# Performance work log

Hardware: AMD Instinct MI355X
Metric: run time of the kernel (lower is better)

The kernel has to match this reference:

```python
import jax, jax.numpy as jnp
import numpy as np

B, T, N, F = 4, 24, 1024, 96
H, HD = 3, 32      # spatial GATConv: 3 heads, head-dim 32 (averaged -> 32 per branch, 3 branches -> 96)
GH, GHD = 4, 24    # GroupedGAT: 4 heads concatenated -> 96
E = 8192           # edges per graph


def setup_inputs() -> dict:
    key = jax.random.key(0)
    ks = jax.random.split(key, 24)
    s_in = 1.0 / np.sqrt(F)
    def gat_params(k):
        k1, k2, k3, k4 = jax.random.split(k, 4)
        return (jax.random.normal(k1, (F, H * HD), jnp.float32) * s_in,
                jax.random.normal(k2, (H, HD), jnp.float32) * 0.1,
                jax.random.normal(k3, (H, HD), jnp.float32) * 0.1,
                jax.random.normal(k4, (H, HD), jnp.float32) * 0.02)
    W_d, al_d, ar_d, b_d = gat_params(ks[3])
    W_m, al_m, ar_m, b_m = gat_params(ks[4])
    W_s, al_s, ar_s, b_s = gat_params(ks[5])
    inp = {
        "input": jax.random.normal(ks[0], (B, T, N, F), jnp.float32),
        "spatial_embedding": jax.random.normal(ks[1], (B, T, N, F), jnp.float32),
        "temporal_embedding": jax.random.normal(ks[2], (B, T, N, F), jnp.float32),
        "src_d": jax.random.randint(ks[6], (E,), 0, N, jnp.int32),
        "dst_d": (jnp.arange(E) % N).astype(jnp.int32),
        "src_m": jax.random.randint(ks[7], (E,), 0, N, jnp.int32),
        "dst_m": (jnp.arange(E) % N).astype(jnp.int32),
        "src_s": jax.random.randint(ks[8], (E,), 0, N, jnp.int32),
        "dst_s": (jnp.arange(E) % N).astype(jnp.int32),
        "W_d": W_d, "al_d": al_d, "ar_d": ar_d, "b_d": b_d,
        "W_m": W_m, "al_m": al_m, "ar_m": ar_m, "b_m": b_m,
        "W_s": W_s, "al_s": al_s, "ar_s": ar_s, "b_s": b_s,
        "Wg": jax.random.normal(ks[9], (F, GH * GHD), jnp.float32) * s_in,
        "agl": jax.random.normal(ks[10], (GH, GHD), jnp.float32) * 0.1,
        "agr": jax.random.normal(ks[11], (GH, GHD), jnp.float32) * 0.1,
        "Wf": jax.random.normal(ks[12], (2 * F, F), jnp.float32) * (1.0 / np.sqrt(2 * F)),
        "bf": jnp.zeros((F,), jnp.float32),
    }
    return inp


def _gat(x, src, dst, W, al, ar, b):
    # x: (N, K, F) node features with K = T*B batched feature slots
    K = x.shape[1]
    h = (x @ W).reshape(N, K, H, HD)                       # (N,K,H,HD)
    el = (h * al).sum(-1)                                  # (N,K,H)
    er = (h * ar).sum(-1)
    e = jax.nn.leaky_relu(el[src] + er[dst], 0.2)          # (E,K,H)
    emax = jax.ops.segment_max(e, dst, num_segments=N)
    emax = jnp.where(jnp.isfinite(emax), emax, 0.0)
    ex = jnp.exp(e - emax[dst])
    denom = jax.ops.segment_sum(ex, dst, num_segments=N)
    alpha = ex / (denom[dst] + 1e-9)                       # edge softmax over incoming edges
    out = jax.ops.segment_sum(h[src] * alpha[..., None], dst, num_segments=N)
    return (out + b).mean(2)                               # average heads -> (N,K,HD)


def reference(input, spatial_embedding, temporal_embedding,
              src_d, dst_d, src_m, dst_m, src_s, dst_s,
              W_d, al_d, ar_d, b_d, W_m, al_m, ar_m, b_m, W_s, al_s, ar_s, b_s,
              Wg, agl, agr, Wf, bf):
    # ---------------- SpatialBlock ----------------
    residual_s = input                                     # input_dim == output_dim
    x_in = input + spatial_embedding
    # torch: input.transpose(0,2).reshape(N,-1,F) -> slot order is (t,b)
    x = jnp.transpose(x_in, (2, 1, 0, 3)).reshape(N, T * B, F)
    xd = _gat(x, src_d, dst_d, W_d, al_d, ar_d, b_d)
    xm = _gat(x, src_m, dst_m, W_m, al_m, ar_m, b_m)
    xs = _gat(x, src_s, dst_s, W_s, al_s, ar_s, b_s)
    x_attn = jnp.concatenate([xd, xm, xs], axis=-1)        # (N, T*B, 3*HD=F)
    # torch: transpose(0,1).reshape(batch,T,N,-1)  (keeps original (t,b) slot order quirk)
    x_attn = jnp.transpose(x_attn, (1, 0, 2)).reshape(B, T, N, F)
    cov0 = spatial_embedding[:, 0]                         # (B,N,F)
    attn_S = jax.nn.softmax(cov0 @ jnp.swapaxes(cov0, 1, 2), axis=2)  # (B,N,N)
    # NOTE: embedding_x branch in SpatialBlock is dead code (out is overwritten); skipped.
    spatial = residual_s + x_attn

    # ---------------- TemporalBlock ----------------
    residual_t = input
    xt = jnp.swapaxes(input, 1, 2).reshape(B * N, T, F)    # (B*N, T, F), index k=b*N+n
    # GroupedGAT: dense multi-head GAT over the T=period_num time steps
    hg = (xt @ Wg).reshape(B * N, T, GH, GHD)
    elg = (hg * agl).sum(-1)                               # (BN,T,GH)
    erg = (hg * agr).sum(-1)
    eg = jax.nn.leaky_relu(elg[:, :, None, :] + erg[:, None, :, :], 0.2)  # (BN,Ti,Tj,GH)
    alphag = jax.nn.softmax(eg, axis=2)
    xg = jnp.einsum('kijh,kjhd->kihd', alphag, hg).reshape(B * N, T, GH * GHD)
    covT = temporal_embedding[:, :, 0]                     # (B,T,F)
    attn_T = jax.nn.softmax(covT @ jnp.swapaxes(covT, 1, 2), axis=1)      # softmax over dim=1 as in torch
    # torch: attn.repeat(N,1,1) paired with x of batch index b*N+n -> uses attn[(b*N+n) % B]
    idx = (jnp.arange(B * N) % B)
    emb = jnp.einsum('kij,kjf->kif', attn_T[idx], xt)      # (BN,T,F)
    xg = xg * jax.nn.sigmoid(emb)
    xg = jnp.swapaxes(xg.reshape(B, N, T, F), 1, 2)        # (B,T,N,F)
    temporal = residual_t + xg

    # ---------------- Fusion ----------------
    z = jax.nn.sigmoid(jnp.concatenate([spatial, temporal], axis=-1) @ Wf + bf)
    out = z * spatial + (1.0 - z) * temporal + input
    return out, attn_S
```

## Files before the change

### kernel.cpp

```cpp
#include <hip/hip_runtime.h>
#include <hip/hip_bf16.h>

typedef long long i64;
typedef __attribute__((ext_vector_type(8))) short short8b;
typedef __attribute__((ext_vector_type(4))) short short4b;
typedef __attribute__((ext_vector_type(4))) float f32x4;

union U8 { short8b v; ushort s[8]; };
union U4 { short4b v; ushort s[4]; };

static __device__ __forceinline__ float bs2f(ushort u) {
    union { unsigned int i; float f; } x; x.i = ((unsigned int)u) << 16; return x.f;
}
static __device__ __forceinline__ ushort f2bs(float f) {
    __hip_bfloat16 h = __float2bfloat16(f);
    return *reinterpret_cast<ushort*>(&h);
}
static __device__ __forceinline__ void mfma_bf16(f32x4& acc, short8b a, short8b b) {
    asm volatile("v_mfma_f32_16x16x32_bf16 %0, %1, %2, %0" : "+v"(acc) : "v"(a), "v"(b));
}
static __device__ __forceinline__ void mfma_fence() {
    asm volatile("s_nop 7\n\ts_nop 7\n\ts_nop 7");
}


__global__ __launch_bounds__(256) void prep_weights_kernel(const float* __restrict__ Wd,
                                                           const float* __restrict__ Wm,
                                                           const float* __restrict__ Ws,
                                                           const float* __restrict__ Wg,
                                                           const float* __restrict__ Wf,
                                                           ushort* __restrict__ wtab) {
    int idx = blockIdx.x * 256 + threadIdx.x;
    if (idx < 36864) {
        int w = idx / 9216, rem = idx - w * 9216;
        int c = rem / 96, k = rem - c * 96;
        const float* Wsrc = (w == 0) ? Wd : (w == 1) ? Wm : (w == 2) ? Ws : Wg;
        wtab[w * 9216 + c * 96 + k] = f2bs(Wsrc[k * 96 + c]);
    } else {
        int rem = idx - 36864;
        int c = rem / 192, k = rem - c * 192;
        wtab[36864 + c * 192 + k] = f2bs(Wf[k * 96 + c]);
    }
}

__global__ __launch_bounds__(256) void build_x_kernel(const float* __restrict__ inp,
                                                      const float* __restrict__ spat,
                                                      ushort* __restrict__ x) {
    int i4 = blockIdx.x * 256 + threadIdx.x;
    int q = i4 % 24;
    int r = i4 / 24;
    int n = r & 1023, bt = r >> 10;
    int t = bt % 24, b = bt / 24;
    int k = t * 4 + b;
    float4 a = ((const float4*)inp)[i4];
    float4 s = ((const float4*)spat)[i4];
    U4 u;
    u.s[0] = f2bs(a.x + s.x); u.s[1] = f2bs(a.y + s.y);
    u.s[2] = f2bs(a.z + s.z); u.s[3] = f2bs(a.w + s.w);
    *(short4b*)&x[((i64)((k << 10) | n)) * 96 + q * 4] = u.v;
}

__global__ __launch_bounds__(256) void gemm96_mfma_kernel(const ushort* __restrict__ X,
                                                          const ushort* __restrict__ wt,
                                                          ushort* __restrict__ Ho) {
    __shared__ ushort Xs[128 * 104];
    __shared__ ushort Wt[96 * 104];
    int tid = threadIdx.x;
    i64 row0 = (i64)blockIdx.x * 128;
    for (int i = tid; i < 1152; i += 256) {
        int c = i / 12, kg = i - c * 12;
        *(short8b*)&Wt[c * 104 + kg * 8] = *(const short8b*)&wt[c * 96 + kg * 8];
    }
    for (int i = tid; i < 1536; i += 256) {
        int r = i / 12, q = i - r * 12;
        *(short8b*)&Xs[r * 104 + q * 8] = *(const short8b*)&X[(row0 + r) * 96 + q * 8];
    }
    __syncthreads();
    int wid = tid >> 6, lane = tid & 63;
    int lr = lane & 15, lk = lane >> 4;
    f32x4 acc[2][6];
#pragma unroll
    for (int m = 0; m < 2; ++m)
#pragma unroll
        for (int c = 0; c < 6; ++c) acc[m][c] = (f32x4){0.f, 0.f, 0.f, 0.f};
    const ushort* xa = &Xs[(wid * 32 + lr) * 104 + lk * 8];
    const ushort* wb = &Wt[lr * 104 + lk * 8];
#pragma unroll
    for (int ks = 0; ks < 3; ++ks) {
        short8b a0 = *(const short8b*)(xa + ks * 32);
        short8b a1 = *(const short8b*)(xa + 16 * 104 + ks * 32);
#pragma unroll
        for (int c = 0; c < 6; ++c) {
            short8b b = *(const short8b*)(wb + c * 16 * 104 + ks * 32);
            mfma_bf16(acc[0][c], a0, b);
            mfma_bf16(acc[1][c], a1, b);
        }
    }
    mfma_fence();
#pragma unroll
    for (int m = 0; m < 2; ++m)
#pragma unroll
        for (int c = 0; c < 6; ++c)
#pragma unroll
            for (int r = 0; r < 4; ++r) {
                i64 row = row0 + wid * 32 + m * 16 + lk * 4 + r;
                Ho[row * 96 + c * 16 + lr] = f2bs(acc[m][c][r]);
            }
}

__global__ __launch_bounds__(256) void gemm96_hg_mfma_kernel(const float* __restrict__ inp,
                                                             const ushort* __restrict__ wt,
                                                             ushort* __restrict__ Ho) {
    __shared__ ushort Xs[128 * 104];
    __shared__ ushort Wt[96 * 104];
    int tid = threadIdx.x;
    i64 row0 = (i64)blockIdx.x * 128;
    for (int i = tid; i < 1152; i += 256) {
        int c = i / 12, kg = i - c * 12;
        *(short8b*)&Wt[c * 104 + kg * 8] = *(const short8b*)&wt[c * 96 + kg * 8];
    }
    for (int i = tid; i < 3072; i += 256) {
        int r = i / 24, q = i - r * 24;
        int row = (int)row0 + r;
        int kk = row / 24, t = row - kk * 24;
        int b = kk >> 10, n = kk & 1023;
        float4 v = ((const float4*)inp)[((i64)(((b * 24 + t) << 10) | n)) * 24 + q];
        U4 u;
        u.s[0] = f2bs(v.x); u.s[1] = f2bs(v.y); u.s[2] = f2bs(v.z); u.s[3] = f2bs(v.w);
        *(short4b*)&Xs[r * 104 + q * 4] = u.v;
    }
    __syncthreads();
    int wid = tid >> 6, lane = tid & 63;
    int lr = lane & 15, lk = lane >> 4;
    f32x4 acc[2][6];
#pragma unroll
    for (int m = 0; m < 2; ++m)
#pragma unroll
        for (int c = 0; c < 6; ++c) acc[m][c] = (f32x4){0.f, 0.f, 0.f, 0.f};
    const ushort* xa = &Xs[(wid * 32 + lr) * 104 + lk * 8];
    const ushort* wb = &Wt[lr * 104 + lk * 8];
#pragma unroll
    for (int ks = 0; ks < 3; ++ks) {
        short8b a0 = *(const short8b*)(xa + ks * 32);
        short8b a1 = *(const short8b*)(xa + 16 * 104 + ks * 32);
#pragma unroll
        for (int c = 0; c < 6; ++c) {
            short8b b = *(const short8b*)(wb + c * 16 * 104 + ks * 32);
            mfma_bf16(acc[0][c], a0, b);
            mfma_bf16(acc[1][c], a1, b);
        }
    }
    mfma_fence();
#pragma unroll
    for (int m = 0; m < 2; ++m)
#pragma unroll
        for (int c = 0; c < 6; ++c)
#pragma unroll
            for (int r = 0; r < 4; ++r) {
                i64 row = row0 + wid * 32 + m * 16 + lk * 4 + r;
                Ho[row * 96 + c * 16 + lr] = f2bs(acc[m][c][r]);
            }
}

__global__ __launch_bounds__(256) void eler_kernel(const ushort* __restrict__ H2,
                                                   const float* __restrict__ al,
                                                   const float* __restrict__ ar,
                                                   float* __restrict__ el,
                                                   float* __restrict__ er) {
    int idx = blockIdx.x * 256 + threadIdx.x;
    int kn = idx / 3, h = idx - kn * 3;
    const ushort* hp = H2 + (i64)kn * 96 + h * 32;
    const float* alp = al + h * 32;
    const float* arp = ar + h * 32;
    float a = 0.f, b2 = 0.f;
#pragma unroll
    for (int c8 = 0; c8 < 4; ++c8) {
        short8b v = *(const short8b*)(hp + c8 * 8);
#pragma unroll
        for (int q = 0; q < 8; ++q) {
            float hv = bs2f((ushort)v[q]);
            a += hv * alp[c8 * 8 + q];
            b2 += hv * arp[c8 * 8 + q];
        }
    }
    el[idx] = a;
    er[idx] = b2;
}

__global__ __launch_bounds__(256) void gat_agg_kernel(const ushort* __restrict__ H2,
                                                      const float* __restrict__ el,
                                                      const float* __restrict__ er,
                                                      const int* __restrict__ src,
                                                      const float* __restrict__ bv,
                                                      ushort* __restrict__ xattn,
                                                      int g) {
    int tid = threadIdx.x;
    int pp = tid >> 3, l8 = tid & 7;
    int p = blockIdx.x * 32 + pp;
    int k = p >> 10, n = p & 1023;
    int d0 = l8 * 4;
    int s[8];
#pragma unroll
    for (int j = 0; j < 8; ++j) s[j] = src[n + j * 1024];
    float acc[4] = {0.f, 0.f, 0.f, 0.f};
#pragma unroll
    for (int h = 0; h < 3; ++h) {
        float erv = er[((i64)((k << 10) | n)) * 3 + h];
        float e[8];
        float m = -1e30f;
#pragma unroll
        for (int j = 0; j < 8; ++j) {
            float ev = el[((i64)((k << 10) | s[j])) * 3 + h] + erv;
            ev = ev >= 0.f ? ev : 0.2f * ev;
            e[j] = ev;
            m = fmaxf(m, ev);
        }
        float sum = 0.f;
#pragma unroll
        for (int j = 0; j < 8; ++j) { e[j] = expf(e[j] - m); sum += e[j]; }
        float inv = 1.f / (sum + 1e-9f);
        float o[4] = {0.f, 0.f, 0.f, 0.f};
#pragma unroll
        for (int j = 0; j < 8; ++j) {
            U4 hv; hv.v = *(const short4b*)&H2[((i64)((k << 10) | s[j])) * 96 + h * 32 + d0];
#pragma unroll
            for (int c = 0; c < 4; ++c) o[c] += e[j] * bs2f(hv.s[c]);
        }
#pragma unroll
        for (int c = 0; c < 4; ++c) acc[c] += o[c] * inv + bv[h * 32 + d0 + c];
    }
    U4 u;
#pragma unroll
    for (int c = 0; c < 4; ++c) u.s[c] = f2bs(acc[c] * (1.f / 3.f));
    *(short4b*)&xattn[((i64)((k << 10) | n)) * 96 + g * 32 + d0] = u.v;
}

__global__ __launch_bounds__(256) void attn_scores_kernel(const float* __restrict__ spat,
                                                          float* __restrict__ attnS) {
    int bid = blockIdx.x;
    int b = bid >> 8;
    int i0 = ((bid >> 4) & 15) * 64;
    int j0 = (bid & 15) * 64;
    const float* C = spat + (i64)b * 24 * 1024 * 96;
    __shared__ __align__(16) float As[64 * 100];
    __shared__ __align__(16) float Bs[64 * 100];
    int tid = threadIdx.x;
    float4* As4 = (float4*)As;
    float4* Bs4 = (float4*)Bs;
    const float4* Ai = (const float4*)(C + (i64)i0 * 96);
    const float4* Bj = (const float4*)(C + (i64)j0 * 96);
    for (int i = tid; i < 1536; i += 256) {
        int row = i / 24, q = i - row * 24;
        As4[row * 25 + q] = Ai[i];
        Bs4[row * 25 + q] = Bj[i];
    }
    __syncthreads();
    int tj = tid & 15, ti = tid >> 4;
    float acc[4][4];
#pragma unroll
    for (int r = 0; r < 4; ++r)
#pragma unroll
        for (int s = 0; s < 4; ++s) acc[r][s] = 0.f;
    for (int k4 = 0; k4 < 24; ++k4) {
        float4 a[4], bv[4];
#pragma unroll
        for (int r = 0; r < 4; ++r) a[r] = As4[(ti * 4 + r) * 25 + k4];
#pragma unroll
        for (int s = 0; s < 4; ++s) bv[s] = Bs4[(s * 16 + tj) * 25 + k4];
#pragma unroll
        for (int r = 0; r < 4; ++r)
#pragma unroll
            for (int s = 0; s < 4; ++s)
                acc[r][s] += a[r].x * bv[s].x + a[r].y * bv[s].y + a[r].z * bv[s].z + a[r].w * bv[s].w;
    }
#pragma unroll
    for (int r = 0; r < 4; ++r) {
        i64 orow = ((i64)(b << 10) + i0 + ti * 4 + r) * 1024 + j0;
#pragma unroll
        for (int s = 0; s < 4; ++s) attnS[orow + s * 16 + tj] = acc[r][s];
    }
}

__global__ __launch_bounds__(256) void attn_softmax_kernel(float* __restrict__ attnS) {
    i64 base = (i64)blockIdx.x * 1024;
    float4* row4 = (float4*)(attnS + base);
    int tid = threadIdx.x;
    float4 v = row4[tid];
    __shared__ float red[256];
    float m = fmaxf(fmaxf(v.x, v.y), fmaxf(v.z, v.w));
    red[tid] = m;
    __syncthreads();
    for (int st = 128; st > 0; st >>= 1) {
        if (tid < st) red[tid] = fmaxf(red[tid], red[tid + st]);
        __syncthreads();
    }
    m = red[0];
    __syncthreads();
    v.x = expf(v.x - m); v.y = expf(v.y - m); v.z = expf(v.z - m); v.w = expf(v.w - m);
    red[tid] = v.x + v.y + v.z + v.w;
    __syncthreads();
    for (int st = 128; st > 0; st >>= 1) {
        if (tid < st) red[tid] += red[tid + st];
        __syncthreads();
    }
    float inv = 1.f / red[0];
    v.x *= inv; v.y *= inv; v.z *= inv; v.w *= inv;
    row4[tid] = v;
}

__global__ __launch_bounds__(576) void attn_t_kernel(const float* __restrict__ temp,
                                                     float* __restrict__ attnT) {
    int b = blockIdx.x;
    int tid = threadIdx.x;
    __shared__ float cs[24][96];
    __shared__ float M[24][24];
    for (int i = tid; i < 2304; i += 576) {
        int r = i / 96, f = i - r * 96;
        cs[r][f] = temp[((i64)(b * 24 + r)) * 1024 * 96 + f];
    }
    __syncthreads();
    int i = tid / 24, j = tid - i * 24;
    float s = 0.f;
#pragma unroll
    for (int f = 0; f < 96; ++f) s += cs[i][f] * cs[j][f];
    M[i][j] = s;
    __syncthreads();
    float m = -1e30f;
#pragma unroll
    for (int i2 = 0; i2 < 24; ++i2) m = fmaxf(m, M[i2][j]);
    float sum = 0.f;
#pragma unroll
    for (int i2 = 0; i2 < 24; ++i2) sum += expf(M[i2][j] - m);
    attnT[((i64)b * 24 + i) * 24 + j] = expf(M[i][j] - m) / sum;
}

__global__ __launch_bounds__(192) void temporal_kernel(const float* __restrict__ inp,
                                                       const ushort* __restrict__ hg,
                                                       const float* __restrict__ agl,
                                                       const float* __restrict__ agr,
                                                       const float* __restrict__ attnT,
                                                       ushort* __restrict__ gated) {
    int kk = blockIdx.x;
    int b = kk >> 10, n = kk & 1023;
    __shared__ __align__(16) float hgs[24 * 100];
    __shared__ __align__(16) float xs[24 * 100];
    __shared__ float at[24 * 24];
    __shared__ float elg[24][4], erg[24][4];
    __shared__ float alpha[4][24][24];
    int tid = threadIdx.x;
    for (int i = tid; i < 576; i += 192) {
        int r = i / 24, q = i - r * 24;
        U4 u; u.v = *(const short4b*)&hg[(i64)kk * 2304 + r * 96 + q * 4];
        float4 v;
        v.x = bs2f(u.s[0]); v.y = bs2f(u.s[1]); v.z = bs2f(u.s[2]); v.w = bs2f(u.s[3]);
        *(float4*)&hgs[r * 100 + q * 4] = v;
    }
    for (int i = tid; i < 576; i += 192) {
        int r = i / 24, q = i - r * 24;
        *(float4*)&xs[r * 100 + q * 4] =
            ((const float4*)inp)[(((i64)(b * 24 + r)) << 10 | n) * 24 + q];
    }
    int ib = kk & 3;
    for (int i = tid; i < 576; i += 192) at[i] = attnT[ib * 576 + i];
    __syncthreads();
    if (tid < 96) {
        int i = tid >> 2, g = tid & 3;
        float a = 0.f, r2 = 0.f;
#pragma unroll
        for (int d = 0; d < 24; ++d) {
            float hv = hgs[i * 100 + g * 24 + d];
            a += hv * agl[g * 24 + d];
            r2 += hv * agr[g * 24 + d];
        }
        elg[i][g] = a;
        erg[i][g] = r2;
    }
    __syncthreads();
    if (tid < 96) {
        int i = tid >> 2, g = tid & 3;
        float ev[24];
        float m = -1e30f;
        float eli = elg[i][g];
#pragma unroll
        for (int j = 0; j < 24; ++j) {
            float e = eli + erg[j][g];
            e = e >= 0.f ? e : 0.2f * e;
            ev[j] = e;
            m = fmaxf(m, e);
        }
        float sum = 0.f;
#pragma unroll
        for (int j = 0; j < 24; ++j) { ev[j] = expf(ev[j] - m); sum += ev[j]; }
        float inv = 1.f / sum;
#pragma unroll
        for (int j = 0; j < 24; ++j) alpha[g][i][j] = ev[j] * inv;
    }
    __syncthreads();
#pragma unroll
    for (int s2 = 0; s2 < 3; ++s2) {
        int idx = tid + s2 * 192;
        int i = idx / 24, f4 = idx - i * 24;
        int g = f4 / 6;
        const float* ap = &alpha[g][i][0];
        const float* atp = &at[i * 24];
        float4 xg = {0.f, 0.f, 0.f, 0.f}, emb = {0.f, 0.f, 0.f, 0.f};
#pragma unroll 8
        for (int j = 0; j < 24; ++j) {
            float a = ap[j], w = atp[j];
            float4 h4 = *(const float4*)&hgs[j * 100 + f4 * 4];
            float4 x4 = *(const float4*)&xs[j * 100 + f4 * 4];
            xg.x += a * h4.x; xg.y += a * h4.y; xg.z += a * h4.z; xg.w += a * h4.w;
            emb.x += w * x4.x; emb.y += w * x4.y; emb.z += w * x4.z; emb.w += w * x4.w;
        }
        U4 o;
        o.s[0] = f2bs(xg.x / (1.f + expf(-emb.x)));
        o.s[1] = f2bs(xg.y / (1.f + expf(-emb.y)));
        o.s[2] = f2bs(xg.z / (1.f + expf(-emb.z)));
        o.s[3] = f2bs(xg.w / (1.f + expf(-emb.w)));
        *(short4b*)&gated[(i64)kk * 2304 + i * 96 + f4 * 4] = o.v;
    }
}

__global__ __launch_bounds__(256) void fusion_mfma_kernel(const float* __restrict__ inp,
                                                          const ushort* __restrict__ xattn,
                                                          const ushort* __restrict__ gated,
                                                          const ushort* __restrict__ wtf,
                                                          const float* __restrict__ bfv,
                                                          float* __restrict__ outb) {
    __shared__ ushort Xs[64 * 200];
    __shared__ ushort Wt[96 * 200];
    int tid = threadIdx.x;
    i64 row0 = (i64)blockIdx.x * 64;
    for (int i = tid; i < 2304; i += 256) {
        int c = i / 24, kg = i - c * 24;
        *(short8b*)&Wt[c * 200 + kg * 8] = *(const short8b*)&wtf[c * 192 + kg * 8];
    }
    for (int i = tid; i < 768; i += 256) {
        int r = i / 12, q = i - r * 12;
        i64 grow = row0 + r;
        int n = (int)(grow & 1023);
        int bt = (int)(grow >> 10);
        int t = bt % 24, b = bt / 24;
        float4 iv0 = ((const float4*)inp)[grow * 24 + q * 2];
        float4 iv1 = ((const float4*)inp)[grow * 24 + q * 2 + 1];
        U8 xa; xa.v = *(const short8b*)&xattn[grow * 96 + q * 8];
        U8 gd; gd.v = *(const short8b*)&gated[(((i64)((b << 10) | n)) * 24 + t) * 96 + q * 8];
        float ivf[8] = {iv0.x, iv0.y, iv0.z, iv0.w, iv1.x, iv1.y, iv1.z, iv1.w};
        U8 sp, tm;
#pragma unroll
        for (int j = 0; j < 8; ++j) {
            sp.s[j] = f2bs(ivf[j] + bs2f(xa.s[j]));
            tm.s[j] = f2bs(ivf[j] + bs2f(gd.s[j]));
        }
        *(short8b*)&Xs[r * 200 + q * 8] = sp.v;
        *(short8b*)&Xs[r * 200 + 96 + q * 8] = tm.v;
    }
    __syncthreads();
    int wid = tid >> 6, lane = tid & 63;
    int lr = lane & 15, lk = lane >> 4;
    f32x4 acc[6];
#pragma unroll
    for (int c = 0; c < 6; ++c) acc[c] = (f32x4){0.f, 0.f, 0.f, 0.f};
    const ushort* xa = &Xs[(wid * 16 + lr) * 200 + lk * 8];
    const ushort* wb = &Wt[lr * 200 + lk * 8];
#pragma unroll
    for (int ks = 0; ks < 6; ++ks) {
        short8b a = *(const short8b*)(xa + ks * 32);
#pragma unroll
        for (int c = 0; c < 6; ++c) {
            short8b b = *(const short8b*)(wb + c * 16 * 200 + ks * 32);
            mfma_bf16(acc[c], a, b);
        }
    }
    mfma_fence();
#pragma unroll
    for (int c = 0; c < 6; ++c) {
        int col = c * 16 + lr;
        float bfc = bfv[col];
#pragma unroll
        for (int r = 0; r < 4; ++r) {
            int lrow = wid * 16 + lk * 4 + r;
            i64 grow = row0 + lrow;
            float z = 1.f / (1.f + expf(-(acc[c][r] + bfc)));
            float sp = bs2f(Xs[lrow * 200 + col]);
            float tm = bs2f(Xs[lrow * 200 + 96 + col]);
            float iv = inp[grow * 96 + col];
            outb[grow * 96 + col] = z * sp + (1.f - z) * tm + iv;
        }
    }
}

extern "C" void kernel_launch(void* const* d_in, const int* in_sizes, int n_in,
                              void* d_out, int out_size, void* d_ws, size_t ws_size,
                              hipStream_t stream) {
    const float* input = (const float*)d_in[0];
    const float* spat  = (const float*)d_in[1];
    const float* temp  = (const float*)d_in[2];
    const int* src_d = (const int*)d_in[3];
    const int* src_m = (const int*)d_in[5];
    const int* src_s = (const int*)d_in[7];
    const float* W_d  = (const float*)d_in[9];
    const float* al_d = (const float*)d_in[10];
    const float* ar_d = (const float*)d_in[11];
    const float* b_d  = (const float*)d_in[12];
    const float* W_m  = (const float*)d_in[13];
    const float* al_m = (const float*)d_in[14];
    const float* ar_m = (const float*)d_in[15];
    const float* b_m  = (const float*)d_in[16];
    const float* W_s  = (const float*)d_in[17];
    const float* al_s = (const float*)d_in[18];
    const float* ar_s = (const float*)d_in[19];
    const float* b_s  = (const float*)d_in[20];
    const float* Wg   = (const float*)d_in[21];
    const float* agl  = (const float*)d_in[22];
    const float* agr  = (const float*)d_in[23];
    const float* Wf   = (const float*)d_in[24];
    const float* bf_  = (const float*)d_in[25];

    float* outb  = (float*)d_out;
    float* attnS = outb + 9437184;

    float* wsf = (float*)d_ws;
    ushort* xbf      = (ushort*)wsf;
    ushort* hgbf     = xbf;
    ushort* H2bf     = (ushort*)(wsf + 4718592);
    ushort* gatedbf  = H2bf;
    ushort* xattnbf  = (ushort*)(wsf + 9437184);
    float* el    = wsf + 14155776;
    float* er    = el + 294912;
    float* attnT = er + 294912;
    ushort* wtab = (ushort*)(wsf + 14747904);
    ushort* wt_d = wtab;
    ushort* wt_m = wtab + 9216;
    ushort* wt_s = wtab + 18432;
    ushort* wtg  = wtab + 27648;
    ushort* wtf  = wtab + 36864;

    prep_weights_kernel<<<216, 256, 0, stream>>>(W_d, W_m, W_s, Wg, Wf, wtab);
    build_x_kernel<<<9216, 256, 0, stream>>>(input, spat, xbf);

    const ushort* Wgat[3] = {wt_d, wt_m, wt_s};
    const float* algat[3] = {al_d, al_m, al_s};
    const float* argat[3] = {ar_d, ar_m, ar_s};
    const float* bgat[3] = {b_d, b_m, b_s};
    const int* srcs[3] = {src_d, src_m, src_s};
    for (int g = 0; g < 3; ++g) {
        gemm96_mfma_kernel<<<768, 256, 0, stream>>>(xbf, Wgat[g], H2bf);
        eler_kernel<<<1152, 256, 0, stream>>>(H2bf, algat[g], argat[g], el, er);
        gat_agg_kernel<<<3072, 256, 0, stream>>>(H2bf, el, er, srcs[g], bgat[g],
                                                 xattnbf, g);
    }

    attn_scores_kernel<<<1024, 256, 0, stream>>>(spat, attnS);
    attn_softmax_kernel<<<4096, 256, 0, stream>>>(attnS);

    gemm96_hg_mfma_kernel<<<768, 256, 0, stream>>>(input, wtg, hgbf);
    attn_t_kernel<<<4, 576, 0, stream>>>(temp, attnT);
    temporal_kernel<<<4096, 192, 0, stream>>>(input, hgbf, agl, agr, attnT, gatedbf);
    fusion_mfma_kernel<<<1536, 256, 0, stream>>>(input, xattnbf, gatedbf, wtf, bf_, outb);
}
```

Before: 297.3 us.

## Fold attention-logit projections into the GEMM weights as extra output columns

Precomputes W·a_l and W·a_r as extra weight columns, so the spatial and temporal projection GEMMs emit the el/er logits directly from a seventh MFMA column tile. This removes the three eler_kernel launches and their rereads of the bf16 H tensors, plus the per-block logit dot products in temporal_kernel. In exchange each GEMM does about 1/6 more MFMA work, and the logits are now computed from bf16-rounded folded weights rather than from bf16 H, which shifts numerics slightly. The workspace layout is rearranged so the temporal logit buffers reuse the el region.

```diff
diff --git a/kernel.cpp b/kernel.cpp
--- a/kernel.cpp
+++ b/kernel.cpp
@@ -24,22 +24,47 @@
 }
 
 
-__global__ __launch_bounds__(256) void prep_weights_kernel(const float* __restrict__ Wd,
-                                                           const float* __restrict__ Wm,
-                                                           const float* __restrict__ Ws,
-                                                           const float* __restrict__ Wg,
-                                                           const float* __restrict__ Wf,
-                                                           ushort* __restrict__ wtab) {
+__global__ __launch_bounds__(256) void prep_weights_kernel(
+        const float* __restrict__ Wd, const float* __restrict__ Wm,
+        const float* __restrict__ Ws, const float* __restrict__ Wg,
+        const float* __restrict__ Wf,
+        const float* __restrict__ ald, const float* __restrict__ ard,
+        const float* __restrict__ alm, const float* __restrict__ arm,
+        const float* __restrict__ als, const float* __restrict__ ars,
+        const float* __restrict__ agl, const float* __restrict__ agr,
+        ushort* __restrict__ wtab) {
     int idx = blockIdx.x * 256 + threadIdx.x;
-    if (idx < 36864) {
-        int w = idx / 9216, rem = idx - w * 9216;
+    if (idx >= 61440) return;
+    if (idx < 43008) {
+        int w = idx / 10752, rem = idx - w * 10752;
         int c = rem / 96, k = rem - c * 96;
-        const float* Wsrc = (w == 0) ? Wd : (w == 1) ? Wm : (w == 2) ? Ws : Wg;
-        wtab[w * 9216 + c * 96 + k] = f2bs(Wsrc[k * 96 + c]);
+        float v;
+        if (w < 3) {
+            const float* W = (w == 0) ? Wd : (w == 1) ? Wm : Ws;
+            if (c < 96) {
+                v = W[k * 96 + c];
+            } else {
+                int j = c - 96, h = j >> 1;
+                const float* a = (j & 1) ? ((w == 0) ? ard : (w == 1) ? arm : ars)
+                                         : ((w == 0) ? ald : (w == 1) ? alm : als);
+                v = 0.f;
+                for (int d = 0; d < 32; ++d) v += W[k * 96 + h * 32 + d] * a[h * 32 + d];
+            }
+        } else {
+            if (c < 96) {
+                v = Wg[k * 96 + c];
+            } else {
+                int j = c - 96, g = j & 3;
+                const float* a = (j >> 2) ? agr : agl;
+                v = 0.f;
+                for (int d = 0; d < 24; ++d) v += Wg[k * 96 + g * 24 + d] * a[g * 24 + d];
+            }
+        }
+        wtab[w * 10752 + c * 96 + k] = f2bs(v);
     } else {
-        int rem = idx - 36864;
+        int rem = idx - 43008;
         int c = rem / 192, k = rem - c * 192;
-        wtab[36864 + c * 192 + k] = f2bs(Wf[k * 96 + c]);
+        wtab[43008 + c * 192 + k] = f2bs(Wf[k * 96 + c]);
     }
 }
 
@@ -62,12 +87,14 @@
 
 __global__ __launch_bounds__(256) void gemm96_mfma_kernel(const ushort* __restrict__ X,
                                                           const ushort* __restrict__ wt,
-                                                          ushort* __restrict__ Ho) {
+                                                          ushort* __restrict__ Ho,
+                                                          float* __restrict__ el,
+                                                          float* __restrict__ er) {
     __shared__ ushort Xs[128 * 104];
-    __shared__ ushort Wt[96 * 104];
+    __shared__ ushort Wt[112 * 104];
     int tid = threadIdx.x;
     i64 row0 = (i64)blockIdx.x * 128;
-    for (int i = tid; i < 1152; i += 256) {
+    for (int i = tid; i < 1344; i += 256) {
         int c = i / 12, kg = i - c * 12;
         *(short8b*)&Wt[c * 104 + kg * 8] = *(const short8b*)&wt[c * 96 + kg * 8];
     }
@@ -78,11 +105,11 @@
     __syncthreads();
     int wid = tid >> 6, lane = tid & 63;
     int lr = lane & 15, lk = lane >> 4;
-    f32x4 acc[2][6];
+    f32x4 acc[2][7];
 #pragma unroll
     for (int m = 0; m < 2; ++m)
 #pragma unroll
-        for (int c = 0; c < 6; ++c) acc[m][c] = (f32x4){0.f, 0.f, 0.f, 0.f};
+        for (int c = 0; c < 7; ++c) acc[m][c] = (f32x4){0.f, 0.f, 0.f, 0.f};
     const ushort* xa = &Xs[(wid * 32 + lr) * 104 + lk * 8];
     const ushort* wb = &Wt[lr * 104 + lk * 8];
 #pragma unroll
@@ -90,7 +117,7 @@
         short8b a0 = *(const short8b*)(xa + ks * 32);
         short8b a1 = *(const short8b*)(xa + 16 * 104 + ks * 32);
 #pragma unroll
-        for (int c = 0; c < 6; ++c) {
+        for (int c = 0; c < 7; ++c) {
             short8b b = *(const short8b*)(wb + c * 16 * 104 + ks * 32);
             mfma_bf16(acc[0][c], a0, b);
             mfma_bf16(acc[1][c], a1, b);
@@ -98,7 +125,7 @@
     }
     mfma_fence();
 #pragma unroll
-    for (int m = 0; m < 2; ++m)
+    for (int m = 0; m < 2; ++m) {
 #pragma unroll
         for (int c = 0; c < 6; ++c)
 #pragma unroll
@@ -106,16 +133,28 @@
                 i64 row = row0 + wid * 32 + m * 16 + lk * 4 + r;
                 Ho[row * 96 + c * 16 + lr] = f2bs(acc[m][c][r]);
             }
+        if (lr < 6) {
+            float* dst = (lr & 1) ? er : el;
+            int h = lr >> 1;
+#pragma unroll
+            for (int r = 0; r < 4; ++r) {
+                i64 row = row0 + wid * 32 + m * 16 + lk * 4 + r;
+                dst[row * 3 + h] = acc[m][6][r];
+            }
+        }
+    }
 }
 
 __global__ __launch_bounds__(256) void gemm96_hg_mfma_kernel(const float* __restrict__ inp,
                                                              const ushort* __restrict__ wt,
-                                                             ushort* __restrict__ Ho) {
+                                                             ushort* __restrict__ Ho,
+                                                             float* __restrict__ elg,
+                                                             float* __restrict__ erg) {
     __shared__ ushort Xs[128 * 104];
-    __shared__ ushort Wt[96 * 104];
+    __shared__ ushort Wt[112 * 104];
     int tid = threadIdx.x;
     i64 row0 = (i64)blockIdx.x * 128;
-    for (int i = tid; i < 1152; i += 256) {
+    for (int i = tid; i < 1344; i += 256) {
         int c = i / 12, kg = i - c * 12;
         *(short8b*)&Wt[c * 104 + kg * 8] = *(const short8b*)&wt[c * 96 + kg * 8];
     }
@@ -132,11 +171,11 @@
     __syncthreads();
     int wid = tid >> 6, lane = tid & 63;
     int lr = lane & 15, lk = lane >> 4;
-    f32x4 acc[2][6];
+    f32x4 acc[2][7];
 #pragma unroll
     for (int m = 0; m < 2; ++m)
 #pragma unroll
-        for (int c = 0; c < 6; ++c) acc[m][c] = (f32x4){0.f, 0.f, 0.f, 0.f};
+        for (int c = 0; c < 7; ++c) acc[m][c] = (f32x4){0.f, 0.f, 0.f, 0.f};
     const ushort* xa = &Xs[(wid * 32 + lr) * 104 + lk * 8];
     const ushort* wb = &Wt[lr * 104 + lk * 8];
 #pragma unroll
@@ -144,7 +183,7 @@
         short8b a0 = *(const short8b*)(xa + ks * 32);
         short8b a1 = *(const short8b*)(xa + 16 * 104 + ks * 32);
 #pragma unroll
-        for (int c = 0; c < 6; ++c) {
+        for (int c = 0; c < 7; ++c) {
             short8b b = *(const short8b*)(wb + c * 16 * 104 + ks * 32);
             mfma_bf16(acc[0][c], a0, b);
             mfma_bf16(acc[1][c], a1, b);
@@ -152,7 +191,7 @@
     }
     mfma_fence();
 #pragma unroll
-    for (int m = 0; m < 2; ++m)
+    for (int m = 0; m < 2; ++m) {
 #pragma unroll
         for (int c = 0; c < 6; ++c)
 #pragma unroll
@@ -160,31 +199,16 @@
                 i64 row = row0 + wid * 32 + m * 16 + lk * 4 + r;
                 Ho[row * 96 + c * 16 + lr] = f2bs(acc[m][c][r]);
             }
-}
-
-__global__ __launch_bounds__(256) void eler_kernel(const ushort* __restrict__ H2,
-                                                   const float* __restrict__ al,
-                                                   const float* __restrict__ ar,
-                                                   float* __restrict__ el,
-                                                   float* __restrict__ er) {
-    int idx = blockIdx.x * 256 + threadIdx.x;
-    int kn = idx / 3, h = idx - kn * 3;
-    const ushort* hp = H2 + (i64)kn * 96 + h * 32;
-    const float* alp = al + h * 32;
-    const float* arp = ar + h * 32;
-    float a = 0.f, b2 = 0.f;
-#pragma unroll
-    for (int c8 = 0; c8 < 4; ++c8) {
-        short8b v = *(const short8b*)(hp + c8 * 8);
-#pragma unroll
-        for (int q = 0; q < 8; ++q) {
-            float hv = bs2f((ushort)v[q]);
-            a += hv * alp[c8 * 8 + q];
-            b2 += hv * arp[c8 * 8 + q];
-        }
-    }
-    el[idx] = a;
-    er[idx] = b2;
+        if (lr < 8) {
+            float* dst = (lr >> 2) ? erg : elg;
+            int g = lr & 3;
+#pragma unroll
+            for (int r = 0; r < 4; ++r) {
+                i64 row = row0 + wid * 32 + m * 16 + lk * 4 + r;
+                dst[row * 4 + g] = acc[m][6][r];
+            }
+        }
+    }
 }
 
 __global__ __launch_bounds__(256) void gat_agg_kernel(const ushort* __restrict__ H2,
@@ -336,8 +360,8 @@
 
 __global__ __launch_bounds__(192) void temporal_kernel(const float* __restrict__ inp,
                                                        const ushort* __restrict__ hg,
-                                                       const float* __restrict__ agl,
-                                                       const float* __restrict__ agr,
+                                                       const float* __restrict__ elgb,
+                                                       const float* __restrict__ ergb,
                                                        const float* __restrict__ attnT,
                                                        ushort* __restrict__ gated) {
     int kk = blockIdx.x;
@@ -345,7 +369,8 @@
     __shared__ __align__(16) float hgs[24 * 100];
     __shared__ __align__(16) float xs[24 * 100];
     __shared__ float at[24 * 24];
-    __shared__ float elg[24][4], erg[24][4];
+    __shared__ __align__(16) float elg[24][4];
+    __shared__ __align__(16) float erg[24][4];
     __shared__ float alpha[4][24][24];
     int tid = threadIdx.x;
     for (int i = tid; i < 576; i += 192) {
@@ -362,18 +387,10 @@
     }
     int ib = kk & 3;
     for (int i = tid; i < 576; i += 192) at[i] = attnT[ib * 576 + i];
-    __syncthreads();
-    if (tid < 96) {
-        int i = tid >> 2, g = tid & 3;
-        float a = 0.f, r2 = 0.f;
-#pragma unroll
-        for (int d = 0; d < 24; ++d) {
-            float hv = hgs[i * 100 + g * 24 + d];
-            a += hv * agl[g * 24 + d];
-            r2 += hv * agr[g * 24 + d];
-        }
-        elg[i][g] = a;
-        erg[i][g] = r2;
+    for (int i = tid; i < 48; i += 192) {
+        int r = i >> 1;
+        if (i & 1) *(float4*)&erg[r][0] = ((const float4*)ergb)[(i64)kk * 24 + r];
+        else       *(float4*)&elg[r][0] = ((const float4*)elgb)[(i64)kk * 24 + r];
     }
     __syncthreads();
     if (tid < 96) {
@@ -528,25 +545,26 @@
     ushort* xattnbf  = (ushort*)(wsf + 9437184);
     float* el    = wsf + 14155776;
     float* er    = el + 294912;
-    float* attnT = er + 294912;
-    ushort* wtab = (ushort*)(wsf + 14747904);
+    float* elgb  = wsf + 14155776;
+    float* attnT = wsf + 14745600;
+    float* ergb  = wsf + 14747904;
+    ushort* wtab = (ushort*)(wsf + 15141120);
     ushort* wt_d = wtab;
-    ushort* wt_m = wtab + 9216;
-    ushort* wt_s = wtab + 18432;
-    ushort* wtg  = wtab + 27648;
-    ushort* wtf  = wtab + 36864;
-
-    prep_weights_kernel<<<216, 256, 0, stream>>>(W_d, W_m, W_s, Wg, Wf, wtab);
+    ushort* wt_m = wtab + 10752;
+    ushort* wt_s = wtab + 21504;
+    ushort* wtg  = wtab + 32256;
+    ushort* wtf  = wtab + 43008;
+
+    prep_weights_kernel<<<240, 256, 0, stream>>>(W_d, W_m, W_s, Wg, Wf,
+                                                 al_d, ar_d, al_m, ar_m, al_s, ar_s,
+                                                 agl, agr, wtab);
     build_x_kernel<<<9216, 256, 0, stream>>>(input, spat, xbf);
 
     const ushort* Wgat[3] = {wt_d, wt_m, wt_s};
-    const float* algat[3] = {al_d, al_m, al_s};
-    const float* argat[3] = {ar_d, ar_m, ar_s};
     const float* bgat[3] = {b_d, b_m, b_s};
     const int* srcs[3] = {src_d, src_m, src_s};
     for (int g = 0; g < 3; ++g) {
-        gemm96_mfma_kernel<<<768, 256, 0, stream>>>(xbf, Wgat[g], H2bf);
-        eler_kernel<<<1152, 256, 0, stream>>>(H2bf, algat[g], argat[g], el, er);
+        gemm96_mfma_kernel<<<768, 256, 0, stream>>>(xbf, Wgat[g], H2bf, el, er);
         gat_agg_kernel<<<3072, 256, 0, stream>>>(H2bf, el, er, srcs[g], bgat[g],
                                                  xattnbf, g);
     }
@@ -554,8 +572,8 @@
     attn_scores_kernel<<<1024, 256, 0, stream>>>(spat, attnS);
     attn_softmax_kernel<<<4096, 256, 0, stream>>>(attnS);
 
-    gemm96_hg_mfma_kernel<<<768, 256, 0, stream>>>(input, wtg, hgbf);
+    gemm96_hg_mfma_kernel<<<768, 256, 0, stream>>>(input, wtg, hgbf, elgb, ergb);
     attn_t_kernel<<<4, 576, 0, stream>>>(temp, attnT);
-    temporal_kernel<<<4096, 192, 0, stream>>>(input, hgbf, agl, agr, attnT, gatedbf);
+    temporal_kernel<<<4096, 192, 0, stream>>>(input, hgbf, elgb, ergb, attnT, gatedbf);
     fusion_mfma_kernel<<<1536, 256, 0, stream>>>(input, xattnbf, gatedbf, wtf, bf_, outb);
 }
```

New measurement: 272.1 us. -8.5%, faster.
